# Performance work log

Measured on AMD Instinct MI355X. Metric: run time of the kernel, lower is better.

## Reference

```python
import jax, jax.numpy as jnp
import numpy as np

B, T = 512, 200          # batch (trials), time bins
N = 10000                # n_neurons
SI, DI = 100, 68         # static / dynamic input sizes
HS, HD = 256, 128        # hidden_dim_static / hidden_dim_dynamic
K = 1                    # output_size
D = 2 * HD + HS          # 512, routed-GEMM contraction dim


def setup_inputs() -> dict:
    key = jax.random.key(0)
    ks = jax.random.split(key, 19)
    g = lambda i, shape, s=0.05: (jax.random.normal(ks[i], shape, jnp.float32) * s)
    return dict(
        x_static=g(0, (B, SI), 1.0),
        x_dynamic=g(1, (B, T, DI), 1.0),
        neuron_order=jax.random.randint(ks[2], (B,), 0, N),
        w_s1=g(3, (HS, SI)), b_s1=g(4, (HS,)),
        w_s2=g(5, (HS, HS)), b_s2=g(6, (HS,)),
        w_dyn=g(7, (HD, DI)), b_dyn=g(8, (HD,)),
        w_ih_f=g(9, (HD, HD)), w_hh_f=g(10, (HD, HD)),
        b_ih_f=g(11, (HD,)), b_hh_f=g(12, (HD,)),
        w_ih_b=g(13, (HD, HD)), w_hh_b=g(14, (HD, HD)),
        b_ih_b=g(15, (HD,)), b_hh_b=g(16, (HD,)),
        neuron_weights=g(17, (N, D, K)),
        neuron_bias=g(18, (N, 1, K)),
    )


def _rnn_dir(x, w_ih, w_hh, b_ih, b_hh, reverse):
    # x: [B,T,H] -> outputs [B,T,H]; torch nn.RNN with nonlinearity='relu'
    xw = jnp.einsum('bth,oh->bto', x, w_ih) + b_ih + b_hh  # precompute input proj
    h0 = jnp.zeros((x.shape[0], w_hh.shape[0]), x.dtype)

    def step(h, xt):
        h = jax.nn.relu(xt + h @ w_hh.T)
        return h, h

    _, ys = jax.lax.scan(step, h0, jnp.swapaxes(xw, 0, 1), reverse=reverse)
    return jnp.swapaxes(ys, 0, 1)


def reference(x_static, x_dynamic, neuron_order,
              w_s1, b_s1, w_s2, b_s2, w_dyn, b_dyn,
              w_ih_f, w_hh_f, b_ih_f, b_hh_f,
              w_ih_b, w_hh_b, b_ih_b, b_hh_b,
              neuron_weights, neuron_bias):
    # static branch (dropout in eval mode -> identity)
    s = jax.nn.relu(x_static @ w_s1.T + b_s1)
    s = jax.nn.relu(s @ w_s2.T + b_s2)                      # [B,HS]
    # dynamic branch
    d = jax.nn.relu(jnp.einsum('bti,oi->bto', x_dynamic, w_dyn) + b_dyn)  # [B,T,HD]
    fwd = _rnn_dir(d, w_ih_f, w_hh_f, b_ih_f, b_hh_f, reverse=False)
    bwd = _rnn_dir(d, w_ih_b, w_hh_b, b_ih_b, b_hh_b, reverse=True)
    d = jax.nn.relu(jnp.concatenate([fwd, bwd], axis=-1))   # [B,T,2*HD]
    # tile static over time and concat
    s_t = jnp.broadcast_to(s[:, None, :], (s.shape[0], d.shape[1], s.shape[1]))
    final_input = jnp.concatenate([s_t, d], axis=-1)        # [B,T,D]
    # per-sample neuron weight gather + routed batched matmul + bias + ReLU
    Wn = neuron_weights[neuron_order]                       # [B,D,K]
    bn = neuron_bias[neuron_order]                          # [B,1,K]
    out = jnp.einsum('btd,bdk->btk', final_input, Wn) + bn  # [B,T,K]
    return jax.nn.relu(jnp.squeeze(out, -1))                # [B,T] (K=1)
```

## Files before the change

### kernel.cpp

```cpp
#include <hip/hip_runtime.h>
#include <cstdint>

constexpr int B = 512, T = 200, SI = 100, DI = 68, HS = 256, HD = 128, D = 512;
constexpr int BT = B * T;
constexpr int NT = BT / 64;

typedef __attribute__((ext_vector_type(8))) short short8;
typedef __attribute__((ext_vector_type(4))) float floatx4;
typedef _Float16 half8 __attribute__((ext_vector_type(8)));
typedef _Float16 half2t __attribute__((ext_vector_type(2)));
typedef unsigned int uint2v __attribute__((ext_vector_type(2)));
typedef unsigned int uint4v __attribute__((ext_vector_type(4)));

#define DEV __device__ __forceinline__

DEV unsigned short f2bf(float f) {
    unsigned int x = __builtin_bit_cast(unsigned int, f);
    x += 0x7fffu + ((x >> 16) & 1u);
    return (unsigned short)(x >> 16);
}
DEV unsigned int pkbf(float a, float b) {
    return (unsigned int)f2bf(a) | ((unsigned int)f2bf(b) << 16);
}
DEV unsigned short f2h(float f) {
    return __builtin_bit_cast(unsigned short, (_Float16)f);
}
DEV half2t u2h2(unsigned int u) { return __builtin_bit_cast(half2t, u); }
DEV unsigned int pkh(float a, float b) {
    return __builtin_bit_cast(unsigned int, __builtin_amdgcn_cvt_pkrtz(a, b));
}
#if __has_builtin(__builtin_amdgcn_permlane32_swap) && __has_builtin(__builtin_amdgcn_permlane16_swap)
DEV void pl32swap(unsigned int& a, unsigned int& b) {
    uint2v r = __builtin_amdgcn_permlane32_swap(a, b, false, false);
    a = r[0]; b = r[1];
}
DEV void pl16swap(unsigned int& a, unsigned int& b) {
    uint2v r = __builtin_amdgcn_permlane16_swap(a, b, false, false);
    a = r[0]; b = r[1];
}
#else
DEV void pl32swap(unsigned int& a, unsigned int& b) {
    unsigned int na, nb;
    asm("v_mov_b32 %0, %2\n\t"
        "v_mov_b32 %1, %3\n\t"
        "v_permlane32_swap_b32 %0, %1"
        : "=&v"(na), "=&v"(nb) : "v"(a), "v"(b));
    a = na; b = nb;
}
DEV void pl16swap(unsigned int& a, unsigned int& b) {
    unsigned int na, nb;
    asm("v_mov_b32 %0, %2\n\t"
        "v_mov_b32 %1, %3\n\t"
        "v_permlane16_swap_b32 %0, %1"
        : "=&v"(na), "=&v"(nb) : "v"(a), "v"(b));
    a = na; b = nb;
}
#endif

__global__ __launch_bounds__(256) void k_prep(
    const float* __restrict__ wdyn,
    const float* __restrict__ wihf, const float* __restrict__ wihb,
    const float* __restrict__ whhf, const float* __restrict__ whhb,
    const float* __restrict__ bihf, const float* __restrict__ bhhf,
    const float* __restrict__ bihb, const float* __restrict__ bhhb,
    unsigned short* __restrict__ wdyn_bf, unsigned short* __restrict__ wih_bf,
    unsigned short* __restrict__ whh_h, float* __restrict__ bsum)
{
    int gid = blockIdx.x * 256 + threadIdx.x, gs = gridDim.x * 256;
    for (int i = gid; i < HD * 96; i += gs) {
        int r = i / 96, c = i - r * 96;
        wdyn_bf[i] = (c < DI) ? f2bf(wdyn[r * DI + c]) : 0;
    }
    for (int i = gid; i < 2 * HD * HD; i += gs) {
        const float* src = (i < HD * HD) ? wihf : wihb;
        wih_bf[i] = f2bf(src[i & (HD * HD - 1)]);
    }
    for (int i = gid; i < 2 * HD * HD; i += gs) {
        const float* src = (i < HD * HD) ? whhf : whhb;
        whh_h[i] = f2h(src[i & (HD * HD - 1)]);
    }
    for (int i = gid; i < 2 * HD; i += gs) {
        int z = i >> 7, n = i & (HD - 1);
        bsum[i] = z ? (bihb[n] + bhhb[n]) : (bihf[n] + bhhf[n]);
    }
}

__global__ __launch_bounds__(256) void k_static(
    const float* __restrict__ xs_g, const float* __restrict__ w1,
    const float* __restrict__ b1, const float* __restrict__ w2,
    const float* __restrict__ b2, const int* __restrict__ norder,
    const float* __restrict__ nw, const float* __restrict__ nb,
    float* __restrict__ statd)
{
    __shared__ __align__(16) float xs[SI];
    __shared__ __align__(16) float s1[HS];
    __shared__ __align__(16) float red[256];
    int b = blockIdx.x, t = threadIdx.x;
    if (t < SI) xs[t] = xs_g[b * SI + t];
    __syncthreads();
    float a = b1[t];
    const float4* w = (const float4*)(w1 + t * SI);
    const float4* xp4 = (const float4*)xs;
    #pragma unroll
    for (int i = 0; i < SI / 4; ++i) {
        float4 ww = w[i]; float4 xx = xp4[i];
        a += xx.x * ww.x + xx.y * ww.y + xx.z * ww.z + xx.w * ww.w;
    }
    s1[t] = fmaxf(a, 0.f);
    __syncthreads();
    float a2 = b2[t];
    const float4* w2p = (const float4*)(w2 + t * HS);
    const float4* s1p = (const float4*)s1;
    #pragma unroll 8
    for (int i = 0; i < HS / 4; ++i) {
        float4 ww = w2p[i]; float4 s = s1p[i];
        a2 += s.x * ww.x + s.y * ww.y + s.z * ww.z + s.w * ww.w;
    }
    float sv = fmaxf(a2, 0.f);
    int n = norder[b];
    red[t] = sv * nw[(size_t)n * D + t];
    __syncthreads();
    for (int s = 128; s > 0; s >>= 1) {
        if (t < s) red[t] += red[t + s];
        __syncthreads();
    }
    if (t == 0) statd[b] = red[0] + nb[n];
}

__global__ __launch_bounds__(256, 1) void k_dxw(
    const float* __restrict__ xd,
    const unsigned short* __restrict__ wdyn_bf, const float* __restrict__ bdyn,
    const unsigned short* __restrict__ wih_bf, const float* __restrict__ bsum,
    unsigned short* __restrict__ xw)
{
    __shared__ __align__(16) unsigned short xb[64][104];
    __shared__ __align__(16) unsigned short dl[64][136];
    int tid = threadIdx.x;
    int lane = tid & 63, w = tid >> 6;
    int ln = lane & 15, q = lane >> 4;

    short8 wdf[8][3];
    #pragma unroll
    for (int j = 0; j < 8; ++j)
        #pragma unroll
        for (int c = 0; c < 3; ++c)
            wdf[j][c] = *(const short8*)(wdyn_bf + (size_t)(j * 16 + ln) * 96 + c * 32 + q * 8);
    short8 wif[2][8][4];
    #pragma unroll
    for (int z = 0; z < 2; ++z)
        #pragma unroll
        for (int j = 0; j < 8; ++j)
            #pragma unroll
            for (int c = 0; c < 4; ++c)
                wif[z][j][c] = *(const short8*)(wih_bf + (size_t)z * HD * HD +
                    (size_t)(j * 16 + ln) * HD + c * 32 + q * 8);

    for (int i = tid; i < 64 * 104 / 8; i += 256)
        ((uint4v*)xb)[i] = uint4v{0u, 0u, 0u, 0u};

    auto stage = [&](int tile) {
        int R0 = tile * 64;
        for (int i = tid; i < 64 * 17; i += 256) {
            int r = i / 17, c = i - r * 17;
            float4 v = *(const float4*)(xd + (size_t)(R0 + r) * DI + c * 4);
            uint2 pk;
            pk.x = pkbf(v.x, v.y);
            pk.y = pkbf(v.z, v.w);
            *(uint2*)&xb[r][c * 4] = pk;
        }
    };

    stage(blockIdx.x);
    __syncthreads();

    for (int tile = blockIdx.x; tile < NT; tile += gridDim.x) {
        int R0 = tile * 64;
        short8 xf[3];
        #pragma unroll
        for (int c = 0; c < 3; ++c)
            xf[c] = *(const short8*)&xb[w * 16 + ln][c * 32 + q * 8];
        #pragma unroll
        for (int j = 0; j < 8; ++j) {
            floatx4 a = {0.f, 0.f, 0.f, 0.f};
            #pragma unroll
            for (int c = 0; c < 3; ++c)
                a = __builtin_amdgcn_mfma_f32_16x16x32_bf16(wdf[j][c], xf[c], a, 0, 0, 0);
            float4 bd4 = *(const float4*)(bdyn + j * 16 + q * 4);
            uint2 pk;
            pk.x = pkbf(fmaxf(a[0] + bd4.x, 0.f), fmaxf(a[1] + bd4.y, 0.f));
            pk.y = pkbf(fmaxf(a[2] + bd4.z, 0.f), fmaxf(a[3] + bd4.w, 0.f));
            *(uint2*)&dl[w * 16 + ln][j * 16 + q * 4] = pk;
        }
        __syncthreads();

        int nxt = tile + gridDim.x;
        if (nxt < NT) stage(nxt);
        short8 df[4];
        #pragma unroll
        for (int c = 0; c < 4; ++c)
            df[c] = *(const short8*)&dl[w * 16 + ln][c * 32 + q * 8];
        int row = R0 + w * 16 + ln;
        #pragma unroll
        for (int z = 0; z < 2; ++z) {
            unsigned short* outp = xw + (size_t)z * BT * HD;
            #pragma unroll
            for (int j = 0; j < 8; ++j) {
                floatx4 a = {0.f, 0.f, 0.f, 0.f};
                #pragma unroll
                for (int c = 0; c < 4; ++c)
                    a = __builtin_amdgcn_mfma_f32_16x16x32_bf16(wif[z][j][c], df[c], a, 0, 0, 0);
                float4 b4 = *(const float4*)(bsum + z * HD + j * 16 + q * 4);
                uint2 hp;
                hp.x = (unsigned int)f2h(a[0] + b4.x) | ((unsigned int)f2h(a[1] + b4.y) << 16);
                hp.y = (unsigned int)f2h(a[2] + b4.z) | ((unsigned int)f2h(a[3] + b4.w) << 16);
                *(uint2*)(outp + (size_t)row * HD + j * 16 + q * 4) = hp;
            }
        }
        __syncthreads();
    }
}

__global__ __launch_bounds__(512, 1) void k_scan(
    const unsigned short* __restrict__ xw, const unsigned short* __restrict__ whh_h,
    const int* __restrict__ norder, const float* __restrict__ nw,
    float* __restrict__ accf, float* __restrict__ accb)
{
    __shared__ __align__(16) uint4v hxch[2][4][64];

    int tid = threadIdx.x, w = tid >> 6, l = tid & 63, ln = l & 15, q = l >> 4;
    int dir = blockIdx.x >> 5, b0 = (blockIdx.x & 31) * 16;
    const unsigned short* whh = whh_h + (size_t)dir * HD * HD;
    float* acc = (dir ? accb : accf) + (size_t)w * BT;
    int segoff = dir ? (HS + HD) : HS;

    half8 wfr[4];
    #pragma unroll
    for (int c = 0; c < 4; ++c)
        wfr[c] = *(const half8*)(whh + (size_t)(w * 16 + ln) * HD + c * 32 + q * 8);

    int nrow = norder[b0 + ln];
    float4 wnl = *(const float4*)(nw + (size_t)nrow * D + segoff + w * 16 + q * 4);

    half8 hf[4];
    uint4v zz = {0u, 0u, 0u, 0u};
    #pragma unroll
    for (int c = 0; c < 4; ++c) hf[c] = __builtin_bit_cast(half8, zz);

    const unsigned short* xp = xw + ((size_t)dir * BT + (size_t)(b0 + ln) * T) * HD
                               + w * 16 + q * 4;
    float* accp = acc + (size_t)(b0 + ln) * T;
    int tstart = dir ? (T - 1) : 0, dt = dir ? -1 : 1;

    int wc = w >> 1;
    int qp = 2 * (w & 1) + (q >> 1);
    int boff = (q & 1) * 8;

    uint2 x0, x1, x2, x3;
    auto ld = [&](uint2& xb, int idx) {
        xb = *(const uint2*)(xp + (size_t)(tstart + dt * idx) * HD);
    };
    auto step = [&](uint2& xc, int idx) {
        int t = tstart + dt * idx;
        int par = idx & 1;
        half2t lo = u2h2(xc.x), hi = u2h2(xc.y);
        floatx4 a0 = {(float)lo[0], (float)lo[1], (float)hi[0], (float)hi[1]};
        floatx4 a1 = {0.f, 0.f, 0.f, 0.f};
        a0 = __builtin_amdgcn_mfma_f32_16x16x32_f16(wfr[0], hf[0], a0, 0, 0, 0);
        a1 = __builtin_amdgcn_mfma_f32_16x16x32_f16(wfr[1], hf[1], a1, 0, 0, 0);
        a0 = __builtin_amdgcn_mfma_f32_16x16x32_f16(wfr[2], hf[2], a0, 0, 0, 0);
        a1 = __builtin_amdgcn_mfma_f32_16x16x32_f16(wfr[3], hf[3], a1, 0, 0, 0);
        floatx4 a = a0 + a1;
        float r0 = fmaxf(a[0], 0.f), r1 = fmaxf(a[1], 0.f);
        float r2 = fmaxf(a[2], 0.f), r3 = fmaxf(a[3], 0.f);
        uint2 hp;
        hp.x = pkh(r0, r1);
        hp.y = pkh(r2, r3);
        *(uint2*)((char*)&hxch[par][wc][qp * 16 + ln] + boff) = hp;
        float p = r0 * wnl.x + r1 * wnl.y + r2 * wnl.z + r3 * wnl.w;
        unsigned int pa = __builtin_bit_cast(unsigned int, p), pb = pa;
        pl32swap(pa, pb);
        float ps = __builtin_bit_cast(float, pa) + __builtin_bit_cast(float, pb);
        unsigned int pc = __builtin_bit_cast(unsigned int, ps), pd = pc;
        pl16swap(pc, pd);
        float ptot = __builtin_bit_cast(float, pc) + __builtin_bit_cast(float, pd);
        if (l < 16) accp[t] = ptot;
        asm volatile("s_waitcnt lgkmcnt(0)" ::: "memory");
        __builtin_amdgcn_sched_barrier(0);
        __builtin_amdgcn_s_barrier();
        __builtin_amdgcn_sched_barrier(0);
        #pragma unroll
        for (int c = 0; c < 4; ++c)
            hf[c] = __builtin_bit_cast(half8, hxch[par][c][l]);
    };

    ld(x0, 0); ld(x1, 1); ld(x2, 2); ld(x3, 3);
    for (int c = 0; c < T / 4 - 1; ++c) {
        int i0 = c * 4;
        step(x0, i0);     ld(x0, i0 + 4);
        step(x1, i0 + 1); ld(x1, i0 + 5);
        step(x2, i0 + 2); ld(x2, i0 + 6);
        step(x3, i0 + 3); ld(x3, i0 + 7);
    }
    step(x0, T - 4);
    step(x1, T - 3);
    step(x2, T - 2);
    step(x3, T - 1);
}

__global__ __launch_bounds__(256) void k_final(
    const float* __restrict__ statd, const float* __restrict__ accf,
    const float* __restrict__ accb, float* __restrict__ out)
{
    int idx = blockIdx.x * 256 + threadIdx.x;
    if (idx < BT) {
        int b = idx / T;
        float s = statd[b];
        #pragma unroll
        for (int w = 0; w < 8; ++w)
            s += accf[(size_t)w * BT + idx] + accb[(size_t)w * BT + idx];
        out[idx] = fmaxf(s, 0.f);
    }
}

extern "C" void kernel_launch(void* const* d_in, const int* in_sizes, int n_in,
                              void* d_out, int out_size, void* d_ws, size_t ws_size,
                              hipStream_t stream)
{
    const float* x_static  = (const float*)d_in[0];
    const float* x_dynamic = (const float*)d_in[1];
    const int*   norder    = (const int*)d_in[2];
    const float* w_s1   = (const float*)d_in[3];
    const float* b_s1   = (const float*)d_in[4];
    const float* w_s2   = (const float*)d_in[5];
    const float* b_s2   = (const float*)d_in[6];
    const float* w_dyn  = (const float*)d_in[7];
    const float* b_dyn  = (const float*)d_in[8];
    const float* w_ih_f = (const float*)d_in[9];
    const float* w_hh_f = (const float*)d_in[10];
    const float* b_ih_f = (const float*)d_in[11];
    const float* b_hh_f = (const float*)d_in[12];
    const float* w_ih_b = (const float*)d_in[13];
    const float* w_hh_b = (const float*)d_in[14];
    const float* b_ih_b = (const float*)d_in[15];
    const float* b_hh_b = (const float*)d_in[16];
    const float* nw     = (const float*)d_in[17];
    const float* nb     = (const float*)d_in[18];
    float* out = (float*)d_out;

    char* ws = (char*)d_ws;
    float* statd = (float*)ws;
    float* accf  = (float*)(ws + 2048);
    float* accb  = (float*)(ws + 2048 + (size_t)8 * BT * 4);
    unsigned short* xw = (unsigned short*)(ws + 2048 + (size_t)16 * BT * 4);
    size_t xw_bytes = (size_t)2 * BT * HD * 2;
    unsigned short* wdyn_bf = (unsigned short*)(ws + 2048 + (size_t)16 * BT * 4 + xw_bytes);
    unsigned short* wih_bf  = wdyn_bf + HD * 96;
    unsigned short* whh_h   = wih_bf + 2 * HD * HD;
    float* bsum = (float*)(whh_h + 2 * HD * HD);

    hipLaunchKernelGGL(k_prep, dim3(64), dim3(256), 0, stream,
                       w_dyn, w_ih_f, w_ih_b, w_hh_f, w_hh_b,
                       b_ih_f, b_hh_f, b_ih_b, b_hh_b,
                       wdyn_bf, wih_bf, whh_h, bsum);
    hipLaunchKernelGGL(k_static, dim3(B), dim3(256), 0, stream,
                       x_static, w_s1, b_s1, w_s2, b_s2, norder, nw, nb, statd);
    hipLaunchKernelGGL(k_dxw, dim3(256), dim3(256), 0, stream,
                       x_dynamic, wdyn_bf, b_dyn, wih_bf, bsum, xw);
    hipLaunchKernelGGL(k_scan, dim3(64), dim3(512), 0, stream,
                       xw, whh_h, norder, nw, accf, accb);
    hipLaunchKernelGGL(k_final, dim3((BT + 255) / 256), dim3(256), 0, stream,
                       statd, accf, accb, out);
}
```

Measured before the change: 244.5 us.

## Fuse prep with static branch and scan with final reduction, merge scan directions

Merges the weight-prep kernel into the static-branch kernel (512 blocks) and folds the final sum/ReLU into the scan kernel. The scan now runs both directions for a 16-batch slice in one 1024-thread block (32 blocks instead of 64), so each block can finish its output rows after a block barrier. This removes two launches and their gaps, but halves the number of scan blocks/CUs used and raises per-block register pressure, which may slow the latency-bound recurrence.

Result: slower. 316.8 us (+29.6%).

```diff
diff --git a/kernel.cpp b/kernel.cpp
--- a/kernel.cpp
+++ b/kernel.cpp
@@ -57,60 +57,58 @@
 }
 #endif
 
-__global__ __launch_bounds__(256) void k_prep(
+__global__ __launch_bounds__(256) void k_prep_static(
     const float* __restrict__ wdyn,
     const float* __restrict__ wihf, const float* __restrict__ wihb,
     const float* __restrict__ whhf, const float* __restrict__ whhb,
     const float* __restrict__ bihf, const float* __restrict__ bhhf,
     const float* __restrict__ bihb, const float* __restrict__ bhhb,
     unsigned short* __restrict__ wdyn_bf, unsigned short* __restrict__ wih_bf,
-    unsigned short* __restrict__ whh_h, float* __restrict__ bsum)
-{
-    int gid = blockIdx.x * 256 + threadIdx.x, gs = gridDim.x * 256;
-    for (int i = gid; i < HD * 96; i += gs) {
-        int r = i / 96, c = i - r * 96;
-        wdyn_bf[i] = (c < DI) ? f2bf(wdyn[r * DI + c]) : 0;
-    }
-    for (int i = gid; i < 2 * HD * HD; i += gs) {
-        const float* src = (i < HD * HD) ? wihf : wihb;
-        wih_bf[i] = f2bf(src[i & (HD * HD - 1)]);
-    }
-    for (int i = gid; i < 2 * HD * HD; i += gs) {
-        const float* src = (i < HD * HD) ? whhf : whhb;
-        whh_h[i] = f2h(src[i & (HD * HD - 1)]);
-    }
-    for (int i = gid; i < 2 * HD; i += gs) {
-        int z = i >> 7, n = i & (HD - 1);
-        bsum[i] = z ? (bihb[n] + bhhb[n]) : (bihf[n] + bhhf[n]);
-    }
-}
-
-__global__ __launch_bounds__(256) void k_static(
+    unsigned short* __restrict__ whh_h, float* __restrict__ bsum,
     const float* __restrict__ xs_g, const float* __restrict__ w1,
     const float* __restrict__ b1, const float* __restrict__ w2,
     const float* __restrict__ b2, const int* __restrict__ norder,
     const float* __restrict__ nw, const float* __restrict__ nb,
     float* __restrict__ statd)
 {
-    __shared__ __align__(16) float xs[SI];
-    __shared__ __align__(16) float s1[HS];
-    __shared__ __align__(16) float red[256];
-    int b = blockIdx.x, t = threadIdx.x;
-    if (t < SI) xs[t] = xs_g[b * SI + t];
-    __syncthreads();
-    float a = b1[t];
-    const float4* w = (const float4*)(w1 + t * SI);
-    const float4* xp4 = (const float4*)xs;
+    int tid = threadIdx.x;
+    int gid = blockIdx.x * 256 + tid, gs = gridDim.x * 256;
+    for (int i = gid; i < HD * 96; i += gs) {
+        int r = i / 96, c = i - r * 96;
+        wdyn_bf[i] = (c < DI) ? f2bf(wdyn[r * DI + c]) : 0;
+    }
+    for (int i = gid; i < 2 * HD * HD; i += gs) {
+        const float* src = (i < HD * HD) ? wihf : wihb;
+        wih_bf[i] = f2bf(src[i & (HD * HD - 1)]);
+    }
+    for (int i = gid; i < 2 * HD * HD; i += gs) {
+        const float* src = (i < HD * HD) ? whhf : whhb;
+        whh_h[i] = f2h(src[i & (HD * HD - 1)]);
+    }
+    for (int i = gid; i < 2 * HD; i += gs) {
+        int z = i >> 7, n = i & (HD - 1);
+        bsum[i] = z ? (bihb[n] + bhhb[n]) : (bihf[n] + bhhf[n]);
+    }
+
+    __shared__ __align__(16) float sxs[104];
+    __shared__ __align__(16) float ss1[HS];
+    __shared__ __align__(16) float sred[256];
+    int b = blockIdx.x;
+    if (tid < SI) sxs[tid] = xs_g[b * SI + tid];
+    __syncthreads();
+    float a = b1[tid];
+    const float4* wr  = (const float4*)(w1 + tid * SI);
+    const float4* xp4 = (const float4*)sxs;
     #pragma unroll
     for (int i = 0; i < SI / 4; ++i) {
-        float4 ww = w[i]; float4 xx = xp4[i];
+        float4 ww = wr[i]; float4 xx = xp4[i];
         a += xx.x * ww.x + xx.y * ww.y + xx.z * ww.z + xx.w * ww.w;
     }
-    s1[t] = fmaxf(a, 0.f);
-    __syncthreads();
-    float a2 = b2[t];
-    const float4* w2p = (const float4*)(w2 + t * HS);
-    const float4* s1p = (const float4*)s1;
+    ss1[tid] = fmaxf(a, 0.f);
+    __syncthreads();
+    float a2 = b2[tid];
+    const float4* w2p = (const float4*)(w2 + tid * HS);
+    const float4* s1p = (const float4*)ss1;
     #pragma unroll 8
     for (int i = 0; i < HS / 4; ++i) {
         float4 ww = w2p[i]; float4 s = s1p[i];
@@ -118,13 +116,13 @@
     }
     float sv = fmaxf(a2, 0.f);
     int n = norder[b];
-    red[t] = sv * nw[(size_t)n * D + t];
+    sred[tid] = sv * nw[(size_t)n * D + tid];
     __syncthreads();
     for (int s = 128; s > 0; s >>= 1) {
-        if (t < s) red[t] += red[t + s];
+        if (tid < s) sred[tid] += sred[tid + s];
         __syncthreads();
     }
-    if (t == 0) statd[b] = red[0] + nb[n];
+    if (tid == 0) statd[b] = sred[0] + nb[n];
 }
 
 __global__ __launch_bounds__(256, 1) void k_dxw(
@@ -220,26 +218,32 @@
     }
 }
 
-__global__ __launch_bounds__(512, 1) void k_scan(
+__global__ __launch_bounds__(1024, 1) void k_scan_final(
     const unsigned short* __restrict__ xw, const unsigned short* __restrict__ whh_h,
     const int* __restrict__ norder, const float* __restrict__ nw,
-    float* __restrict__ accf, float* __restrict__ accb)
+    float* __restrict__ accf, float* __restrict__ accb,
+    const float* __restrict__ statd, float* __restrict__ out)
 {
-    __shared__ __align__(16) uint4v hxch[2][4][64];
-
-    int tid = threadIdx.x, w = tid >> 6, l = tid & 63, ln = l & 15, q = l >> 4;
-    int dir = blockIdx.x >> 5, b0 = (blockIdx.x & 31) * 16;
+    __shared__ __align__(16) uint4v hxch[2][2][4][64];
+
+    int tid = threadIdx.x;
+    int wvall = tid >> 6;
+    int dir = wvall >> 3;
+    int wv = wvall & 7;
+    int l = tid & 63, ln = l & 15, q = l >> 4;
+    int b0 = blockIdx.x * 16;
+
     const unsigned short* whh = whh_h + (size_t)dir * HD * HD;
-    float* acc = (dir ? accb : accf) + (size_t)w * BT;
+    float* accp = (dir ? accb : accf) + (size_t)wv * BT + (size_t)(b0 + ln) * T;
     int segoff = dir ? (HS + HD) : HS;
 
     half8 wfr[4];
     #pragma unroll
     for (int c = 0; c < 4; ++c)
-        wfr[c] = *(const half8*)(whh + (size_t)(w * 16 + ln) * HD + c * 32 + q * 8);
+        wfr[c] = *(const half8*)(whh + (size_t)(wv * 16 + ln) * HD + c * 32 + q * 8);
 
     int nrow = norder[b0 + ln];
-    float4 wnl = *(const float4*)(nw + (size_t)nrow * D + segoff + w * 16 + q * 4);
+    float4 wnl = *(const float4*)(nw + (size_t)nrow * D + segoff + wv * 16 + q * 4);
 
     half8 hf[4];
     uint4v zz = {0u, 0u, 0u, 0u};
@@ -247,12 +251,11 @@
     for (int c = 0; c < 4; ++c) hf[c] = __builtin_bit_cast(half8, zz);
 
     const unsigned short* xp = xw + ((size_t)dir * BT + (size_t)(b0 + ln) * T) * HD
-                               + w * 16 + q * 4;
-    float* accp = acc + (size_t)(b0 + ln) * T;
+                               + wv * 16 + q * 4;
     int tstart = dir ? (T - 1) : 0, dt = dir ? -1 : 1;
 
-    int wc = w >> 1;
-    int qp = 2 * (w & 1) + (q >> 1);
+    int wc = wv >> 1;
+    int qp = 2 * (wv & 1) + (q >> 1);
     int boff = (q & 1) * 8;
 
     uint2 x0, x1, x2, x3;
@@ -275,7 +278,7 @@
         uint2 hp;
         hp.x = pkh(r0, r1);
         hp.y = pkh(r2, r3);
-        *(uint2*)((char*)&hxch[par][wc][qp * 16 + ln] + boff) = hp;
+        *(uint2*)((char*)&hxch[dir][par][wc][qp * 16 + ln] + boff) = hp;
         float p = r0 * wnl.x + r1 * wnl.y + r2 * wnl.z + r3 * wnl.w;
         unsigned int pa = __builtin_bit_cast(unsigned int, p), pb = pa;
         pl32swap(pa, pb);
@@ -290,7 +293,7 @@
         __builtin_amdgcn_sched_barrier(0);
         #pragma unroll
         for (int c = 0; c < 4; ++c)
-            hf[c] = __builtin_bit_cast(half8, hxch[par][c][l]);
+            hf[c] = __builtin_bit_cast(half8, hxch[dir][par][c][l]);
     };
 
     ld(x0, 0); ld(x1, 1); ld(x2, 2); ld(x3, 3);
@@ -305,20 +308,17 @@
     step(x1, T - 3);
     step(x2, T - 2);
     step(x3, T - 1);
-}
-
-__global__ __launch_bounds__(256) void k_final(
-    const float* __restrict__ statd, const float* __restrict__ accf,
-    const float* __restrict__ accb, float* __restrict__ out)
-{
-    int idx = blockIdx.x * 256 + threadIdx.x;
-    if (idx < BT) {
-        int b = idx / T;
-        float s = statd[b];
+
+    __syncthreads();
+    for (int idx = tid; idx < 16 * T; idx += 1024) {
+        int bb = b0 + idx / T;
+        int tt = idx - (idx / T) * T;
+        size_t o = (size_t)bb * T + tt;
+        float s = statd[bb];
         #pragma unroll
         for (int w = 0; w < 8; ++w)
-            s += accf[(size_t)w * BT + idx] + accb[(size_t)w * BT + idx];
-        out[idx] = fmaxf(s, 0.f);
+            s += accf[(size_t)w * BT + o] + accb[(size_t)w * BT + o];
+        out[o] = fmaxf(s, 0.f);
     }
 }
 
@@ -358,16 +358,14 @@
     unsigned short* whh_h   = wih_bf + 2 * HD * HD;
     float* bsum = (float*)(whh_h + 2 * HD * HD);
 
-    hipLaunchKernelGGL(k_prep, dim3(64), dim3(256), 0, stream,
+    hipLaunchKernelGGL(k_prep_static, dim3(512), dim3(256), 0, stream,
                        w_dyn, w_ih_f, w_ih_b, w_hh_f, w_hh_b,
                        b_ih_f, b_hh_f, b_ih_b, b_hh_b,
-                       wdyn_bf, wih_bf, whh_h, bsum);
-    hipLaunchKernelGGL(k_static, dim3(B), dim3(256), 0, stream,
-                       x_static, w_s1, b_s1, w_s2, b_s2, norder, nw, nb, statd);
+                       wdyn_bf, wih_bf, whh_h, bsum,
+                       x_static, w_s1, b_s1, w_s2, b_s2, norder, nw, nb,
+                       statd);
     hipLaunchKernelGGL(k_dxw, dim3(256), dim3(256), 0, stream,
                        x_dynamic, wdyn_bf, b_dyn, wih_bf, bsum, xw);
-    hipLaunchKernelGGL(k_scan, dim3(64), dim3(512), 0, stream,
-                       xw, whh_h, norder, nw, accf, accb);
-    hipLaunchKernelGGL(k_final, dim3((BT + 255) / 256), dim3(256), 0, stream,
-                       statd, accf, accb, out);
-}
+    hipLaunchKernelGGL(k_scan_final, dim3(32), dim3(1024), 0, stream,
+                       xw, whh_h, norder, nw, accf, accb, statd, out);
+}
```
